# Kernel optimization log

Measured on AMD Instinct MI355X. Metric: run time of the kernel, lower is better.

The kernel has to match this reference:

```python
import jax, jax.numpy as jnp
import numpy as np

H = 768
R = 7  # len(DISCOURSE_RELATIONS)


def setup_inputs() -> dict:
    key = jax.random.key(0)
    ks = jax.random.split(key, 6)
    B, S = 4, 256
    scale = 1.0 / np.sqrt(H)
    return {
        "pooled_outputs": jax.random.normal(ks[0], (B, S, H), dtype=jnp.float32),
        "w_src": jax.random.uniform(ks[1], (H, H), jnp.float32, -scale, scale),
        "b_src": jax.random.uniform(ks[2], (H,), jnp.float32, -scale, scale),
        "w_tgt": jax.random.uniform(ks[3], (H, H), jnp.float32, -scale, scale),
        "b_tgt": jax.random.uniform(ks[4], (H,), jnp.float32, -scale, scale),
        "w_out": jax.random.uniform(ks[5], (R, H), jnp.float32, -scale, scale),
    }


def reference(pooled_outputs, w_src, b_src, w_tgt, b_tgt, w_out):
    # h_src, h_tgt: [B, S, H]
    h_src = jnp.einsum("bsh,kh->bsk", pooled_outputs, w_src) + b_src
    h_tgt = jnp.einsum("bth,kh->btk", pooled_outputs, w_tgt) + b_tgt
    # broadcast add -> [B, S, S, H], tanh, then small-output linear -> [B, S, S, R]
    h = jnp.tanh(h_src[:, :, None, :] + h_tgt[:, None, :, :])
    return jnp.einsum("bsth,rh->bstr", h, w_out)
```

## Files before the change

### kernel.cpp

```cpp
#include <hip/hip_runtime.h>
#include <hip/hip_bf16.h>

#define HD 768
#define SQ 256
#define NB 4
#define RR 7

typedef short bf16x8 __attribute__((ext_vector_type(8)));
typedef float f32x4  __attribute__((ext_vector_type(4)));

__device__ __forceinline__ float fast_tanh(float x) {
  float e = __expf(2.0f * x);
  return 1.0f - 2.0f / (e + 1.0f);
}

__device__ __forceinline__ float pair_tanh(float a, float b) {
  return (a + b) * __builtin_amdgcn_rcpf(fmaf(a, b, 1.0f));
}

__device__ __forceinline__ short f2bf(float x) {
  return (short)__builtin_bit_cast(unsigned short, __float2bfloat16(x));
}

__device__ __forceinline__ void gl_lds16(const void* g, void* l) {
  __builtin_amdgcn_global_load_lds(
      (const __attribute__((address_space(1))) void*)g,
      (__attribute__((address_space(3))) void*)l, 16, 0, 0);
}

__global__ __launch_bounds__(256) void cvt_kernel(
    const float* __restrict__ X, const float* __restrict__ Ws,
    const float* __restrict__ Wt, const float* __restrict__ Wo,
    short* __restrict__ Xb, short* __restrict__ Wsb,
    short* __restrict__ Wtb, short* __restrict__ Wob)
{
  const int NX = NB * SQ * HD / 8;
  const int NW = HD * HD / 8;
  const int NO = 16 * HD / 8;
  int i = blockIdx.x * 256 + threadIdx.x;
  const float* src; short* dst;
  if (i < NX)               { src = X;  dst = Xb; }
  else if (i < NX + NW)     { src = Ws; dst = Wsb; i -= NX; }
  else if (i < NX + 2 * NW) { src = Wt; dst = Wtb; i -= NX + NW; }
  else if (i < NX + 2 * NW + NO) {
    i -= NX + 2 * NW;
    int row = i / (HD / 8);
    bf16x8 r = {};
    if (row < RR) {
      float4 a = *(const float4*)(Wo + (size_t)i * 8);
      float4 b = *(const float4*)(Wo + (size_t)i * 8 + 4);
      r[0] = f2bf(a.x); r[1] = f2bf(a.y); r[2] = f2bf(a.z); r[3] = f2bf(a.w);
      r[4] = f2bf(b.x); r[5] = f2bf(b.y); r[6] = f2bf(b.z); r[7] = f2bf(b.w);
    }
    *(bf16x8*)(Wob + (size_t)i * 8) = r;
    return;
  } else return;
  float4 a = *(const float4*)(src + (size_t)i * 8);
  float4 b = *(const float4*)(src + (size_t)i * 8 + 4);
  bf16x8 r;
  r[0] = f2bf(a.x); r[1] = f2bf(a.y); r[2] = f2bf(a.z); r[3] = f2bf(a.w);
  r[4] = f2bf(b.x); r[5] = f2bf(b.y); r[6] = f2bf(b.z); r[7] = f2bf(b.w);
  *(bf16x8*)(dst + (size_t)i * 8) = r;
}

__global__ __launch_bounds__(256) void cvt_wout(
    const float* __restrict__ Wo, short* __restrict__ Wob)
{
  const int NO = 16 * HD / 8;
  int i = blockIdx.x * 256 + threadIdx.x;
  if (i >= NO) return;
  int row = i / (HD / 8);
  bf16x8 r = {};
  if (row < RR) {
    float4 a = *(const float4*)(Wo + (size_t)i * 8);
    float4 b = *(const float4*)(Wo + (size_t)i * 8 + 4);
    r[0] = f2bf(a.x); r[1] = f2bf(a.y); r[2] = f2bf(a.z); r[3] = f2bf(a.w);
    r[4] = f2bf(b.x); r[5] = f2bf(b.y); r[6] = f2bf(b.z); r[7] = f2bf(b.w);
  }
  *(bf16x8*)(Wob + (size_t)i * 8) = r;
}

__global__ __launch_bounds__(256) void stage1_lds(
    const short* __restrict__ Xb,
    const short* __restrict__ Wsb, const float* __restrict__ bsrc,
    const short* __restrict__ Wtb, const float* __restrict__ btgt,
    float* __restrict__ ta, float* __restrict__ tb)
{
  constexpr int BK = 64;
  const short* W  = blockIdx.z ? Wtb : Wsb;
  const float* bv = blockIdx.z ? btgt : bsrc;
  float* outp     = blockIdx.z ? tb : ta;
  const int row0 = blockIdx.x * 64, col0 = blockIdx.y * 64;

  __shared__ short As[2][64 * BK];
  __shared__ short Bs[2][64 * BK];

  const int tid = threadIdx.x, wave = tid >> 6, lane = tid & 63;
  const int wm = (wave >> 1) * 32, wn = (wave & 1) * 32;

  f32x4 acc[2][2] = {};

  const int G0 = wave * 64 + lane;
  const int r0 = G0 >> 3, g0 = G0 & 7;
  const int G1 = G0 + 256;
  const int r1 = G1 >> 3, g1 = G1 & 7;

  const size_t xo0 = (size_t)(row0 + r0) * HD + ((g0 ^ (r0 & 7)) * 8);
  const size_t xo1 = (size_t)(row0 + r1) * HD + ((g1 ^ (r1 & 7)) * 8);
  const size_t wo0 = (size_t)(col0 + r0) * HD + ((g0 ^ (r0 & 7)) * 8);
  const size_t wo1 = (size_t)(col0 + r1) * HD + ((g1 ^ (r1 & 7)) * 8);
  short* const la0 = (short*)As + (size_t)(wave * 64) * 8;
  short* const la1 = (short*)As + (size_t)(256 + wave * 64) * 8;
  short* const lb0 = (short*)Bs + (size_t)(wave * 64) * 8;
  short* const lb1 = (short*)Bs + (size_t)(256 + wave * 64) * 8;
  constexpr int BUF = 64 * BK;

  gl_lds16(Xb + xo0, la0);
  gl_lds16(Xb + xo1, la1);
  gl_lds16(W + wo0, lb0);
  gl_lds16(W + wo1, lb1);

  int cur = 0;
  for (int k0 = 0; k0 < HD; k0 += BK) {
    __syncthreads();
    if (k0 + BK < HD) {
      int nb = (cur ^ 1) * BUF;
      gl_lds16(Xb + xo0 + k0 + BK, la0 + nb);
      gl_lds16(Xb + xo1 + k0 + BK, la1 + nb);
      gl_lds16(W + wo0 + k0 + BK, lb0 + nb);
      gl_lds16(W + wo1 + k0 + BK, lb1 + nb);
    }
    const short* Ac = (const short*)As + cur * BUF;
    const short* Bc = (const short*)Bs + cur * BUF;

    #pragma unroll
    for (int kkb = 0; kkb < 2; ++kkb) {
      bf16x8 af[2], bw[2];
      const int q = kkb * 4 + (lane >> 4);
      #pragma unroll
      for (int i = 0; i < 2; ++i) {
        int ar = wm + i * 16 + (lane & 15);
        af[i] = *(const bf16x8*)&Ac[ar * BK + ((q ^ (ar & 7)) * 8)];
        int br = wn + i * 16 + (lane & 15);
        bw[i] = *(const bf16x8*)&Bc[br * BK + ((q ^ (br & 7)) * 8)];
      }
      #pragma unroll
      for (int i = 0; i < 2; ++i)
        #pragma unroll
        for (int j = 0; j < 2; ++j)
          acc[i][j] = __builtin_amdgcn_mfma_f32_16x16x32_bf16(af[i], bw[j], acc[i][j], 0, 0, 0);
    }
    cur ^= 1;
  }

  #pragma unroll
  for (int j = 0; j < 2; ++j) {
    int n = col0 + wn + j * 16 + (lane & 15);
    float bb = bv[n];
    #pragma unroll
    for (int i = 0; i < 2; ++i)
      #pragma unroll
      for (int r = 0; r < 4; ++r) {
        int m = row0 + wm + i * 16 + (lane >> 4) * 4 + r;
        outp[(size_t)m * HD + n] = fast_tanh(acc[i][j][r] + bb);
      }
  }
}

__global__ __launch_bounds__(256) void stage1_mfma(
    const float* __restrict__ X,
    const float* __restrict__ Wsrc, const float* __restrict__ bsrc,
    const float* __restrict__ Wtgt, const float* __restrict__ btgt,
    float* __restrict__ ta, float* __restrict__ tb)
{
  constexpr int BK = 64;
  const float* W  = blockIdx.z ? Wtgt : Wsrc;
  const float* bv = blockIdx.z ? btgt : bsrc;
  float* outp     = blockIdx.z ? tb : ta;
  const int row0 = blockIdx.x * 64, col0 = blockIdx.y * 64;

  __shared__ short As[64 * BK];
  __shared__ short Bs[64 * BK];

  const int tid  = threadIdx.x;
  const int wave = tid >> 6, lane = tid & 63;
  const int wm = (wave >> 1) * 32, wn = (wave & 1) * 32;
  f32x4 acc[2][2] = {};
  const int sr = tid >> 2, sq = tid & 3;

  for (int k0 = 0; k0 < HD; k0 += BK) {
    const float* xa = X + (size_t)(row0 + sr) * HD + k0 + sq * 16;
    const float* xw = W + (size_t)(col0 + sr) * HD + k0 + sq * 16;
    float4 a0 = *(const float4*)(xa + 0), a1 = *(const float4*)(xa + 4);
    float4 a2 = *(const float4*)(xa + 8), a3 = *(const float4*)(xa + 12);
    float4 w0 = *(const float4*)(xw + 0), w1 = *(const float4*)(xw + 4);
    float4 w2 = *(const float4*)(xw + 8), w3 = *(const float4*)(xw + 12);
    __syncthreads();
    bf16x8 p;
    p[0]=f2bf(a0.x);p[1]=f2bf(a0.y);p[2]=f2bf(a0.z);p[3]=f2bf(a0.w);
    p[4]=f2bf(a1.x);p[5]=f2bf(a1.y);p[6]=f2bf(a1.z);p[7]=f2bf(a1.w);
    *(bf16x8*)&As[sr * BK + (((sq * 2 + 0) ^ (sr & 7)) * 8)] = p;
    p[0]=f2bf(a2.x);p[1]=f2bf(a2.y);p[2]=f2bf(a2.z);p[3]=f2bf(a2.w);
    p[4]=f2bf(a3.x);p[5]=f2bf(a3.y);p[6]=f2bf(a3.z);p[7]=f2bf(a3.w);
    *(bf16x8*)&As[sr * BK + (((sq * 2 + 1) ^ (sr & 7)) * 8)] = p;
    p[0]=f2bf(w0.x);p[1]=f2bf(w0.y);p[2]=f2bf(w0.z);p[3]=f2bf(w0.w);
    p[4]=f2bf(w1.x);p[5]=f2bf(w1.y);p[6]=f2bf(w1.z);p[7]=f2bf(w1.w);
    *(bf16x8*)&Bs[sr * BK + (((sq * 2 + 0) ^ (sr & 7)) * 8)] = p;
    p[0]=f2bf(w2.x);p[1]=f2bf(w2.y);p[2]=f2bf(w2.z);p[3]=f2bf(w2.w);
    p[4]=f2bf(w3.x);p[5]=f2bf(w3.y);p[6]=f2bf(w3.z);p[7]=f2bf(w3.w);
    *(bf16x8*)&Bs[sr * BK + (((sq * 2 + 1) ^ (sr & 7)) * 8)] = p;
    __syncthreads();

    #pragma unroll
    for (int kkb = 0; kkb < 2; ++kkb) {
      bf16x8 af[2], bw[2];
      const int q = kkb * 4 + (lane >> 4);
      #pragma unroll
      for (int i = 0; i < 2; ++i) {
        int ar = wm + i * 16 + (lane & 15);
        af[i] = *(const bf16x8*)&As[ar * BK + ((q ^ (ar & 7)) * 8)];
        int br = wn + i * 16 + (lane & 15);
        bw[i] = *(const bf16x8*)&Bs[br * BK + ((q ^ (br & 7)) * 8)];
      }
      #pragma unroll
      for (int i = 0; i < 2; ++i)
        #pragma unroll
        for (int j = 0; j < 2; ++j)
          acc[i][j] = __builtin_amdgcn_mfma_f32_16x16x32_bf16(af[i], bw[j], acc[i][j], 0, 0, 0);
    }
  }

  #pragma unroll
  for (int j = 0; j < 2; ++j) {
    int n = col0 + wn + j * 16 + (lane & 15);
    float bb = bv[n];
    #pragma unroll
    for (int i = 0; i < 2; ++i)
      #pragma unroll
      for (int r = 0; r < 4; ++r) {
        int m = row0 + wm + i * 16 + (lane >> 4) * 4 + r;
        outp[(size_t)m * HD + n] = fast_tanh(acc[i][j][r] + bb);
      }
  }
}

__global__ __launch_bounds__(256, 6) void stage2_mfma(
    const float* __restrict__ ta, const float* __restrict__ tb,
    const short* __restrict__ Wob, float* __restrict__ out)
{
  constexpr int HC = 128, LDp = 132, NC = HD / HC;
  const int b  = blockIdx.z;
  const int s0 = blockIdx.y * 8, t0 = blockIdx.x * 16;

  __shared__ float sa[8][LDp];
  __shared__ float sb[16][LDp];

  const int tid = threadIdx.x, wave = tid >> 6, lane = tid & 63;
  const int lg = lane >> 4;
  const int ln = lane & 15;

  f32x4 acc[2] = {};

  const float* taB = ta + ((size_t)b * SQ + s0) * HD;
  const float* tbB = tb + ((size_t)b * SQ + t0) * HD;

  const int sr = tid >> 5, sq = tid & 31;
  const int rba = tid >> 5;

  float4 va  = *(const float4*)(taB + (size_t)sr * HD + sq * 4);
  float4 vb0 = *(const float4*)(tbB + (size_t)rba * HD + sq * 4);
  float4 vb1 = *(const float4*)(tbB + (size_t)(rba + 8) * HD + sq * 4);

  for (int c = 0; c < NC; ++c) {
    *(float4*)&sa[sr][sq * 4]       = va;
    *(float4*)&sb[rba][sq * 4]      = vb0;
    *(float4*)&sb[rba + 8][sq * 4]  = vb1;
    __syncthreads();

    if (c + 1 < NC) {
      va  = *(const float4*)(taB + (size_t)sr * HD + (c + 1) * HC + sq * 4);
      vb0 = *(const float4*)(tbB + (size_t)rba * HD + (c + 1) * HC + sq * 4);
      vb1 = *(const float4*)(tbB + (size_t)(rba + 8) * HD + (c + 1) * HC + sq * 4);
    }

    #pragma unroll
    for (int m = 0; m < 4; ++m) {
      const int kk = m * 32 + lg * 8;
      bf16x8 bfr = *(const bf16x8*)(Wob + (size_t)ln * HD + c * HC + kk);
      float4 q0 = *(const float4*)&sb[ln][kk];
      float4 q1 = *(const float4*)&sb[ln][kk + 4];
      float bvv[8] = {q0.x,q0.y,q0.z,q0.w,q1.x,q1.y,q1.z,q1.w};

      #pragma unroll
      for (int si = 0; si < 2; ++si) {
        const float* ap = &sa[wave * 2 + si][kk];
        float4 a0 = *(const float4*)ap;
        float4 a1 = *(const float4*)(ap + 4);
        float av[8] = {a0.x,a0.y,a0.z,a0.w,a1.x,a1.y,a1.z,a1.w};
        bf16x8 pa;
        #pragma unroll
        for (int j = 0; j < 8; ++j)
          pa[j] = f2bf(pair_tanh(av[j], bvv[j]));
        acc[si] = __builtin_amdgcn_mfma_f32_16x16x32_bf16(pa, bfr, acc[si], 0, 0, 0);
      }
    }
    __syncthreads();
  }

  if (ln < RR) {
    #pragma unroll
    for (int si = 0; si < 2; ++si) {
      int s = s0 + wave * 2 + si;
      float* op = out + (((size_t)b * SQ + s) * SQ + t0 + lg * 4) * RR + ln;
      op[0]      = acc[si][0];
      op[RR]     = acc[si][1];
      op[2 * RR] = acc[si][2];
      op[3 * RR] = acc[si][3];
    }
  }
}

extern "C" void kernel_launch(void* const* d_in, const int* in_sizes, int n_in,
                              void* d_out, int out_size, void* d_ws, size_t ws_size,
                              hipStream_t stream) {
  (void)in_sizes; (void)n_in; (void)out_size;
  const float* X    = (const float*)d_in[0];
  const float* Wsrc = (const float*)d_in[1];
  const float* bsrc = (const float*)d_in[2];
  const float* Wtgt = (const float*)d_in[3];
  const float* btgt = (const float*)d_in[4];
  const float* Wout = (const float*)d_in[5];
  float* out = (float*)d_out;

  float* taF = (float*)d_ws;
  float* tbF = taF + (size_t)NB * SQ * HD;
  const size_t base = (size_t)2 * NB * SQ * HD * sizeof(float);
  short* Xb  = (short*)((char*)d_ws + base);
  short* Wsb = Xb + (size_t)NB * SQ * HD;
  short* Wtb = Wsb + (size_t)HD * HD;
  short* Wob = Wtb + (size_t)HD * HD;
  const size_t need = base +
      ((size_t)NB * SQ * HD + 2 * (size_t)HD * HD + (size_t)16 * HD) * sizeof(short);

  const short* WobUse;
  if (ws_size >= need) {
    const int total_oct = NB*SQ*HD/8 + 2*(HD*HD/8) + 16*HD/8;
    cvt_kernel<<<(total_oct + 255) / 256, 256, 0, stream>>>(
        X, Wsrc, Wtgt, Wout, Xb, Wsb, Wtb, Wob);
    stage1_lds<<<dim3(16, 12, 2), 256, 0, stream>>>(Xb, Wsb, bsrc, Wtb, btgt, taF, tbF);
    WobUse = Wob;
  } else {
    short* WobF = (short*)((char*)d_ws + base);
    cvt_wout<<<6, 256, 0, stream>>>(Wout, WobF);
    stage1_mfma<<<dim3(16, 12, 2), 256, 0, stream>>>(X, Wsrc, bsrc, Wtgt, btgt, taF, tbF);
    WobUse = WobF;
  }
  stage2_mfma<<<dim3(SQ / 16, SQ / 8, NB), 256, 0, stream>>>(taF, tbF, WobUse, out);
}
```

Measured before the change: 115.0 us.

## Halve stage1 row tile and prefetch W_out fragments in stage2

```diff
diff --git a/kernel.cpp b/kernel.cpp
--- a/kernel.cpp
+++ b/kernel.cpp
@@ -86,84 +86,74 @@
     const short* __restrict__ Wtb, const float* __restrict__ btgt,
     float* __restrict__ ta, float* __restrict__ tb)
 {
-  constexpr int BK = 64;
+  constexpr int BK = 64, BM = 32, BN = 64;
   const short* W  = blockIdx.z ? Wtb : Wsb;
   const float* bv = blockIdx.z ? btgt : bsrc;
   float* outp     = blockIdx.z ? tb : ta;
-  const int row0 = blockIdx.x * 64, col0 = blockIdx.y * 64;
-
-  __shared__ short As[2][64 * BK];
-  __shared__ short Bs[2][64 * BK];
+  const int row0 = blockIdx.x * BM, col0 = blockIdx.y * BN;
+
+  __shared__ short As[2][BM * BK];
+  __shared__ short Bs[2][BN * BK];
 
   const int tid = threadIdx.x, wave = tid >> 6, lane = tid & 63;
-  const int wm = (wave >> 1) * 32, wn = (wave & 1) * 32;
-
-  f32x4 acc[2][2] = {};
-
-  const int G0 = wave * 64 + lane;
-  const int r0 = G0 >> 3, g0 = G0 & 7;
-  const int G1 = G0 + 256;
-  const int r1 = G1 >> 3, g1 = G1 & 7;
-
-  const size_t xo0 = (size_t)(row0 + r0) * HD + ((g0 ^ (r0 & 7)) * 8);
-  const size_t xo1 = (size_t)(row0 + r1) * HD + ((g1 ^ (r1 & 7)) * 8);
-  const size_t wo0 = (size_t)(col0 + r0) * HD + ((g0 ^ (r0 & 7)) * 8);
-  const size_t wo1 = (size_t)(col0 + r1) * HD + ((g1 ^ (r1 & 7)) * 8);
-  short* const la0 = (short*)As + (size_t)(wave * 64) * 8;
-  short* const la1 = (short*)As + (size_t)(256 + wave * 64) * 8;
-  short* const lb0 = (short*)Bs + (size_t)(wave * 64) * 8;
-  short* const lb1 = (short*)Bs + (size_t)(256 + wave * 64) * 8;
-  constexpr int BUF = 64 * BK;
-
-  gl_lds16(Xb + xo0, la0);
-  gl_lds16(Xb + xo1, la1);
-  gl_lds16(W + wo0, lb0);
-  gl_lds16(W + wo1, lb1);
+  const int ln = lane & 15, lg = lane >> 4;
+  const int wm = (wave >> 1) * 16, wn = (wave & 1) * 32;
+
+  f32x4 acc[2] = {};
+
+  const int ra = tid >> 3, ga = tid & 7;
+  const size_t xoff = (size_t)(row0 + ra) * HD + ((ga ^ (ra & 7)) * 8);
+  const int rb0 = tid >> 3, gb0 = tid & 7;
+  const int rb1 = (tid + 256) >> 3, gb1 = tid & 7;
+  const size_t wof0 = (size_t)(col0 + rb0) * HD + ((gb0 ^ (rb0 & 7)) * 8);
+  const size_t wof1 = (size_t)(col0 + rb1) * HD + ((gb1 ^ (rb1 & 7)) * 8);
+  short* const laA  = (short*)As + (size_t)(wave * 64) * 8;
+  short* const laB0 = (short*)Bs + (size_t)(wave * 64) * 8;
+  short* const laB1 = (short*)Bs + (size_t)(256 + wave * 64) * 8;
+  constexpr int BUFA = BM * BK, BUFB = BN * BK;
+
+  gl_lds16(Xb + xoff, laA);
+  gl_lds16(W + wof0, laB0);
+  gl_lds16(W + wof1, laB1);
 
   int cur = 0;
   for (int k0 = 0; k0 < HD; k0 += BK) {
     __syncthreads();
     if (k0 + BK < HD) {
-      int nb = (cur ^ 1) * BUF;
-      gl_lds16(Xb + xo0 + k0 + BK, la0 + nb);
-      gl_lds16(Xb + xo1 + k0 + BK, la1 + nb);
-      gl_lds16(W + wo0 + k0 + BK, lb0 + nb);
-      gl_lds16(W + wo1 + k0 + BK, lb1 + nb);
-    }
-    const short* Ac = (const short*)As + cur * BUF;
-    const short* Bc = (const short*)Bs + cur * BUF;
+      gl_lds16(Xb + xoff + k0 + BK, laA + (cur ^ 1) * BUFA);
+      gl_lds16(W + wof0 + k0 + BK, laB0 + (cur ^ 1) * BUFB);
+      gl_lds16(W + wof1 + k0 + BK, laB1 + (cur ^ 1) * BUFB);
+    }
+    const short* Ac = (const short*)As + cur * BUFA;
+    const short* Bc = (const short*)Bs + cur * BUFB;
 
     #pragma unroll
     for (int kkb = 0; kkb < 2; ++kkb) {
-      bf16x8 af[2], bw[2];
-      const int q = kkb * 4 + (lane >> 4);
+      const int q = kkb * 4 + lg;
+      const int ar = wm + ln;
+      bf16x8 af = *(const bf16x8*)&Ac[ar * BK + ((q ^ (ar & 7)) * 8)];
+      bf16x8 bw[2];
       #pragma unroll
       for (int i = 0; i < 2; ++i) {
-        int ar = wm + i * 16 + (lane & 15);
-        af[i] = *(const bf16x8*)&Ac[ar * BK + ((q ^ (ar & 7)) * 8)];
-        int br = wn + i * 16 + (lane & 15);
+        int br = wn + i * 16 + ln;
         bw[i] = *(const bf16x8*)&Bc[br * BK + ((q ^ (br & 7)) * 8)];
       }
       #pragma unroll
       for (int i = 0; i < 2; ++i)
-        #pragma unroll
-        for (int j = 0; j < 2; ++j)
-          acc[i][j] = __builtin_amdgcn_mfma_f32_16x16x32_bf16(af[i], bw[j], acc[i][j], 0, 0, 0);
+        acc[i] = __builtin_amdgcn_mfma_f32_16x16x32_bf16(af, bw[i], acc[i], 0, 0, 0);
     }
     cur ^= 1;
   }
 
   #pragma unroll
   for (int j = 0; j < 2; ++j) {
-    int n = col0 + wn + j * 16 + (lane & 15);
+    int n = col0 + wn + j * 16 + ln;
     float bb = bv[n];
     #pragma unroll
-    for (int i = 0; i < 2; ++i)
-      #pragma unroll
-      for (int r = 0; r < 4; ++r) {
-        int m = row0 + wm + i * 16 + (lane >> 4) * 4 + r;
-        outp[(size_t)m * HD + n] = fast_tanh(acc[i][j][r] + bb);
-      }
+    for (int r = 0; r < 4; ++r) {
+      int m = row0 + wm + lg * 4 + r;
+      outp[(size_t)m * HD + n] = fast_tanh(acc[j][r] + bb);
+    }
   }
 }
 
@@ -244,7 +234,7 @@
   }
 }
 
-__global__ __launch_bounds__(256, 6) void stage2_mfma(
+__global__ __launch_bounds__(256, 5) void stage2_mfma(
     const float* __restrict__ ta, const float* __restrict__ tb,
     const short* __restrict__ Wob, float* __restrict__ out)
 {
@@ -263,6 +253,7 @@
 
   const float* taB = ta + ((size_t)b * SQ + s0) * HD;
   const float* tbB = tb + ((size_t)b * SQ + t0) * HD;
+  const short* wrow = Wob + (size_t)ln * HD + lg * 8;
 
   const int sr = tid >> 5, sq = tid & 31;
   const int rba = tid >> 5;
@@ -270,7 +261,12 @@
   float4 va  = *(const float4*)(taB + (size_t)sr * HD + sq * 4);
   float4 vb0 = *(const float4*)(tbB + (size_t)rba * HD + sq * 4);
   float4 vb1 = *(const float4*)(tbB + (size_t)(rba + 8) * HD + sq * 4);
-
+  bf16x8 bfr[4], bfrN[4];
+  #pragma unroll
+  for (int m = 0; m < 4; ++m)
+    bfr[m] = *(const bf16x8*)(wrow + m * 32);
+
+  #pragma unroll
   for (int c = 0; c < NC; ++c) {
     *(float4*)&sa[sr][sq * 4]       = va;
     *(float4*)&sb[rba][sq * 4]      = vb0;
@@ -281,12 +277,14 @@
       va  = *(const float4*)(taB + (size_t)sr * HD + (c + 1) * HC + sq * 4);
       vb0 = *(const float4*)(tbB + (size_t)rba * HD + (c + 1) * HC + sq * 4);
       vb1 = *(const float4*)(tbB + (size_t)(rba + 8) * HD + (c + 1) * HC + sq * 4);
+      #pragma unroll
+      for (int m = 0; m < 4; ++m)
+        bfrN[m] = *(const bf16x8*)(wrow + (c + 1) * HC + m * 32);
     }
 
     #pragma unroll
     for (int m = 0; m < 4; ++m) {
       const int kk = m * 32 + lg * 8;
-      bf16x8 bfr = *(const bf16x8*)(Wob + (size_t)ln * HD + c * HC + kk);
       float4 q0 = *(const float4*)&sb[ln][kk];
       float4 q1 = *(const float4*)&sb[ln][kk + 4];
       float bvv[8] = {q0.x,q0.y,q0.z,q0.w,q1.x,q1.y,q1.z,q1.w};
@@ -301,10 +299,15 @@
         #pragma unroll
         for (int j = 0; j < 8; ++j)
           pa[j] = f2bf(pair_tanh(av[j], bvv[j]));
-        acc[si] = __builtin_amdgcn_mfma_f32_16x16x32_bf16(pa, bfr, acc[si], 0, 0, 0);
+        acc[si] = __builtin_amdgcn_mfma_f32_16x16x32_bf16(pa, bfr[m], acc[si], 0, 0, 0);
       }
     }
     __syncthreads();
+    if (c + 1 < NC) {
+      #pragma unroll
+      for (int m = 0; m < 4; ++m)
+        bfr[m] = bfrN[m];
+    }
   }
 
   if (ln < RR) {
@@ -347,7 +350,7 @@
     const int total_oct = NB*SQ*HD/8 + 2*(HD*HD/8) + 16*HD/8;
     cvt_kernel<<<(total_oct + 255) / 256, 256, 0, stream>>>(
         X, Wsrc, Wtgt, Wout, Xb, Wsb, Wtb, Wob);
-    stage1_lds<<<dim3(16, 12, 2), 256, 0, stream>>>(Xb, Wsb, bsrc, Wtb, btgt, taF, tbF);
+    stage1_lds<<<dim3(32, 12, 2), 256, 0, stream>>>(Xb, Wsb, bsrc, Wtb, btgt, taF, tbF);
     WobUse = Wob;
   } else {
     short* WobF = (short*)((char*)d_ws + base);
```

Result: no change. 114.8 us (-0.1%).
